# Kernel tuning notes

Hardware: AMD Instinct MI355X
Metric: run time of the kernel (lower is better)

Reference implementation:

```python
import jax, jax.numpy as jnp
import numpy as np
from jax import lax

WINDOW_RADIUS = 8  # model_config['window_radius']


def _layernorm(x, g, b, eps=1e-5):
    mu = jnp.mean(x, axis=-1, keepdims=True)
    var = jnp.var(x, axis=-1, keepdims=True)
    return (x - mu) * lax.rsqrt(var + eps) * g + b


def setup_inputs() -> dict:
    key = jax.random.key(0)
    ks = jax.random.split(key, 8)
    B, T, D = 4, 2048, 1024
    d_b, d_k, KV = 256, 128, 48
    d_in = D + d_b + d_k  # 1408
    s = 1.0 / np.sqrt(D)
    return {
        "h": jax.random.normal(ks[0], (B, T, D), jnp.float32),
        "bound_w": jax.random.normal(ks[1], (D,), jnp.float32) * s,
        "bound_b": jnp.zeros((1,), jnp.float32),
        "conv_w": jax.random.normal(ks[2], (9,), jnp.float32) * (1.0 / 3.0),
        "conv_b": jnp.zeros((1,), jnp.float32),
        "e0": jnp.zeros((d_b,), jnp.float32),
        "e1": jax.random.normal(ks[3], (d_b,), jnp.float32) * 0.02,
        "key_emb": jax.random.normal(ks[4], (KV, d_k), jnp.float32),
        "key_w": jax.random.normal(ks[5], (D, KV), jnp.float32) * s,
        "key_b": jnp.zeros((KV,), jnp.float32),
        "ln_in_g": jnp.ones((d_in,), jnp.float32),
        "ln_in_b": jnp.zeros((d_in,), jnp.float32),
        "film_w": jax.random.normal(ks[6], (d_in, 2 * D), jnp.float32) * (1.0 / np.sqrt(d_in)),
        "film_b": jnp.zeros((2 * D,), jnp.float32),
        "ln_h_g": jnp.ones((D,), jnp.float32),
        "ln_h_b": jnp.zeros((D,), jnp.float32),
    }


def reference(h, bound_w, bound_b, conv_w, conv_b, e0, e1, key_emb, key_w, key_b,
              ln_in_g, ln_in_b, film_w, film_b, ln_h_g, ln_h_b):
    B, T, D = h.shape
    R = WINDOW_RADIUS
    # boundary head + Conv1d(1,1,k,padding=k//2) smoother + sigmoid
    boundary_logits = jnp.einsum('btd,d->bt', h, bound_w) + bound_b[0]  # [B,T]
    kb = conv_w.shape[0]
    sm = lax.conv_general_dilated(boundary_logits[:, None, :], conv_w[None, None, :],
                                  window_strides=(1,), padding=[(kb // 2, kb // 2)])
    b_soft = jax.nn.sigmoid(sm[:, 0, :] + conv_b[0])  # [B,T]
    # key conditioning: softmax over key logits, soft-mix of key embedding table
    key_soft = jax.nn.softmax(jnp.einsum('btd,dk->btk', h, key_w) + key_b, axis=-1)
    ek = jnp.einsum('btk,ke->bte', key_soft, key_emb)  # [B,T,d_k]
    # boundary embedding interpolation
    eb = b_soft[..., None] * e1 + (1.0 - b_soft[..., None]) * e0  # [B,T,d_b]
    # FiLM: concat + LN + Linear -> gamma/beta, modulate LN(h)
    film_in = _layernorm(jnp.concatenate([h, eb, ek], axis=-1), ln_in_g, ln_in_b)
    gb = jnp.einsum('bti,io->bto', film_in, film_w) + film_b  # [B,T,2D]
    gamma, beta = gb[..., :D], gb[..., D:]
    z = _layernorm(h, ln_h_g, ln_h_b) * (1.0 + gamma) + beta  # [B,T,D]
    # local windows: replicate-pad along T, im2col-style gather of width 2R+1
    padded = jnp.pad(h, ((0, 0), (R, R), (0, 0)), mode='edge')  # [B,T+2R,D]
    idx = jnp.arange(T)[:, None] + jnp.arange(2 * R + 1)[None, :]  # [T,W]
    win = padded[:, idx, :]  # [B,T,W,D]
    C = jnp.concatenate([z[:, :, None, :], win], axis=2)  # [B,T,W+1,D]
    return C
```

## Files before the change

kernel.cpp:

```cpp
#include <hip/hip_runtime.h>
#include <math.h>

#define B_    4
#define T_    2048
#define D_    1024
#define DB_   256
#define DKk_  128
#define KV_   48
#define DIN_  1408
#define NT_   (B_ * T_)
#define RAD_  8

#define OFS_BOUND  0
#define OFS_BSOFT  8192
#define OFS_KEY    16384
#define OFS_EK     409600
#define OFS_HSTAT  1458176
#define OFS_BF16   1474560
#define UOFS_AHI   0u
#define UOFS_ALO   11534336u
#define UOFS_BHI   23068672u
#define UOFS_BLO   25952256u

typedef __attribute__((ext_vector_type(8))) short s16x8;
typedef __attribute__((ext_vector_type(4))) float f32x4;

__device__ __forceinline__ unsigned short f2bf(float f) {
    unsigned u; __builtin_memcpy(&u, &f, 4);
    u += 0x7fffu + ((u >> 16) & 1u);
    return (unsigned short)(u >> 16);
}
__device__ __forceinline__ unsigned short f2bf_hi(float f, float* back) {
    unsigned u; __builtin_memcpy(&u, &f, 4);
    u += 0x7fffu + ((u >> 16) & 1u);
    unsigned short h = (unsigned short)(u >> 16);
    unsigned hb = (unsigned)h << 16;
    __builtin_memcpy(back, &hb, 4);
    return h;
}
__device__ __forceinline__ void gload_lds16(const void* g, void* s) {
    __builtin_amdgcn_global_load_lds(
        (const __attribute__((address_space(1))) unsigned int*)g,
        (__attribute__((address_space(3))) unsigned int*)s,
        16, 0, 0);
}

__global__ __launch_bounds__(256) void k_prepw(
    const float* __restrict__ film_w, unsigned short* __restrict__ Bhi,
    unsigned short* __restrict__ Blo)
{
    __shared__ float tile[32][33];
    const int n0 = blockIdx.x * 32;
    const int k0 = blockIdx.y * 32;
    const int tid = threadIdx.x;
    const int c = tid & 31, r0 = tid >> 5;
    #pragma unroll
    for (int i = 0; i < 4; ++i) {
        int r = r0 + i * 8;
        tile[r][c] = film_w[(size_t)(k0 + r) * 2048 + n0 + c];
    }
    __syncthreads();
    #pragma unroll
    for (int i = 0; i < 4; ++i) {
        int rn = r0 + i * 8;
        float f = tile[c][rn];
        float fh;
        unsigned short hs = f2bf_hi(f, &fh);
        unsigned short ls = f2bf(f - fh);
        Bhi[(size_t)(n0 + rn) * 1408 + k0 + c] = hs;
        Blo[(size_t)(n0 + rn) * 1408 + k0 + c] = ls;
    }
}

__global__ __launch_bounds__(256) void k_logits(
    const float* __restrict__ h, const float* __restrict__ bound_w,
    const float* __restrict__ bound_b, const float* __restrict__ key_w,
    const float* __restrict__ key_b, float* __restrict__ ws)
{
    __shared__ float As[32][64];
    __shared__ float Ws[64][64];
    const int tid  = threadIdx.x;
    const int tok0 = blockIdx.x * 32;
    const int c  = tid & 63;
    const int rg = tid >> 6;
    float acc[8] = {0,0,0,0,0,0,0,0};

    for (int kc = 0; kc < 1024; kc += 64) {
        #pragma unroll
        for (int i = 0; i < 8; ++i) {
            int row = rg + 4 * i;
            As[row][c] = h[(size_t)(tok0 + row) * 1024 + kc + c];
        }
        #pragma unroll
        for (int i = 0; i < 12; ++i) {
            int l = tid + 256 * i;
            int r = l / 48, cc = l - r * 48;
            Ws[r][cc] = key_w[(size_t)(kc + r) * 48 + cc];
        }
        if (tid < 64) Ws[tid][48] = bound_w[kc + tid];
        __syncthreads();
        #pragma unroll 8
        for (int kk = 0; kk < 64; ++kk) {
            float w = Ws[kk][c];
            #pragma unroll
            for (int i = 0; i < 8; ++i)
                acc[i] += As[rg * 8 + i][kk] * w;
        }
        __syncthreads();
    }

    if (c < 48) {
        float kb = key_b[c];
        #pragma unroll
        for (int i = 0; i < 8; ++i)
            ws[OFS_KEY + (size_t)(tok0 + rg * 8 + i) * 48 + c] = acc[i] + kb;
    } else if (c == 48) {
        float bb = bound_b[0];
        #pragma unroll
        for (int i = 0; i < 8; ++i)
            ws[OFS_BOUND + tok0 + rg * 8 + i] = acc[i] + bb;
    }
}

__global__ __launch_bounds__(256) void k_conv(
    const float* __restrict__ conv_w, const float* __restrict__ conv_b,
    float* __restrict__ ws)
{
    int id = blockIdx.x * 256 + threadIdx.x;
    if (id >= NT_) return;
    int b = id >> 11, t = id & 2047;
    float s = conv_b[0];
    #pragma unroll
    for (int i = 0; i < 9; ++i) {
        int tt = t + i - 4;
        if (tt >= 0 && tt < T_) s += ws[OFS_BOUND + b * T_ + tt] * conv_w[i];
    }
    ws[OFS_BSOFT + id] = 1.0f / (1.0f + expf(-s));
}

__global__ __launch_bounds__(128) void k_softek(
    const float* __restrict__ key_emb, float* __restrict__ ws)
{
    __shared__ float p[48];
    const int tok = blockIdx.x;
    const int tid = threadIdx.x;
    if (tid < 64) {
        float v = (tid < 48) ? ws[OFS_KEY + (size_t)tok * 48 + tid] : -1e30f;
        float m = v;
        #pragma unroll
        for (int off = 32; off; off >>= 1) m = fmaxf(m, __shfl_xor(m, off, 64));
        float e = (tid < 48) ? expf(v - m) : 0.0f;
        float s = e;
        #pragma unroll
        for (int off = 32; off; off >>= 1) s += __shfl_xor(s, off, 64);
        if (tid < 48) p[tid] = e / s;
    }
    __syncthreads();
    float acc = 0.0f;
    #pragma unroll 8
    for (int k = 0; k < 48; ++k) acc += p[k] * key_emb[k * 128 + tid];
    ws[OFS_EK + (size_t)tok * 128 + tid] = acc;
}

__global__ __launch_bounds__(256) void k_filmin(
    const float* __restrict__ h, const float* __restrict__ e0,
    const float* __restrict__ e1, const float* __restrict__ ln_in_g,
    const float* __restrict__ ln_in_b, float* __restrict__ ws,
    unsigned short* __restrict__ Ahi, unsigned short* __restrict__ Alo)
{
    const int tok = blockIdx.x;
    const int tid = threadIdx.x;
    const float bs = ws[OFS_BSOFT + tok];
    float val[6];
    float s_all = 0.f, ss_all = 0.f, s_h = 0.f, ss_h = 0.f;
    int n = 0;
    for (int j = tid; j < DIN_; j += 256, ++n) {
        float v;
        if (j < 1024)       v = h[(size_t)tok * 1024 + j];
        else if (j < 1280)  { int i = j - 1024; v = bs * e1[i] + (1.0f - bs) * e0[i]; }
        else                v = ws[OFS_EK + (size_t)tok * 128 + (j - 1280)];
        val[n] = v;
        s_all += v; ss_all += v * v;
        if (j < 1024) { s_h += v; ss_h += v * v; }
    }
    #pragma unroll
    for (int off = 32; off; off >>= 1) {
        s_all  += __shfl_down(s_all, off);
        ss_all += __shfl_down(ss_all, off);
        s_h    += __shfl_down(s_h, off);
        ss_h   += __shfl_down(ss_h, off);
    }
    __shared__ float red[4][4];
    const int wid = tid >> 6;
    if ((tid & 63) == 0) {
        red[wid][0] = s_all; red[wid][1] = ss_all;
        red[wid][2] = s_h;   red[wid][3] = ss_h;
    }
    __syncthreads();
    float S   = red[0][0] + red[1][0] + red[2][0] + red[3][0];
    float SS  = red[0][1] + red[1][1] + red[2][1] + red[3][1];
    float Sh  = red[0][2] + red[1][2] + red[2][2] + red[3][2];
    float SSh = red[0][3] + red[1][3] + red[2][3] + red[3][3];
    float mean  = S * (1.0f / 1408.0f);
    float var   = SS * (1.0f / 1408.0f) - mean * mean;
    float rstd  = rsqrtf(var + 1e-5f);
    float mean_h = Sh * (1.0f / 1024.0f);
    float var_h  = SSh * (1.0f / 1024.0f) - mean_h * mean_h;
    float rstd_h = rsqrtf(var_h + 1e-5f);
    if (tid == 0) {
        ws[OFS_HSTAT + tok * 2]     = mean_h;
        ws[OFS_HSTAT + tok * 2 + 1] = rstd_h;
    }
    n = 0;
    for (int j = tid; j < DIN_; j += 256, ++n) {
        float f = (val[n] - mean) * rstd * ln_in_g[j] + ln_in_b[j];
        float fh;
        unsigned short hs = f2bf_hi(f, &fh);
        Ahi[(size_t)tok * 1408 + j] = hs;
        Alo[(size_t)tok * 1408 + j] = f2bf(f - fh);
    }
}

__global__ __launch_bounds__(256) void k_gemm_mfma(
    const unsigned short* __restrict__ Ahi, const unsigned short* __restrict__ Alo,
    const unsigned short* __restrict__ Bhi, const unsigned short* __restrict__ Blo,
    const float* __restrict__ film_b, const float* __restrict__ h,
    const float* __restrict__ hstat, const float* __restrict__ ln_h_g,
    const float* __restrict__ ln_h_b, float* __restrict__ out)
{
    __shared__ __align__(16) char lds[32768];
    const int tid  = threadIdx.x;
    const int m0   = blockIdx.x * 128;
    const int n0   = blockIdx.y * 64;
    const int lane = tid & 63;
    const int wid  = tid >> 6;
    const int wm   = wid >> 1, wn = wid & 1;
    const int lr   = lane & 15;
    const int hi16 = ((lane >> 4) & 3) * 16;
    const int sa   = (lr & 7) << 4;
    const int srow = tid >> 3;
    const int sswz = ((((tid & 7) * 16) ^ ((srow & 7) << 4)) >> 1);
    const int sdst = tid * 16;

    f32x4 accg[4][2] = {};
    f32x4 accb[4][2] = {};

    #pragma unroll
    for (int s = 0; s < 3; ++s) {
        const unsigned short* Ap = (s == 1) ? Alo : Ahi;
        const unsigned short* Bp = (s == 2) ? Blo : Bhi;
        for (int kc = 0; kc < 1408; kc += 64) {
            #pragma unroll
            for (int c = 0; c < 4; ++c)
                gload_lds16(Ap + (size_t)(m0 + srow + c * 32) * 1408 + kc + sswz,
                            lds + c * 4096 + sdst);
            #pragma unroll
            for (int c = 0; c < 2; ++c) {
                gload_lds16(Bp + (size_t)(n0 + srow + c * 32) * 1408 + kc + sswz,
                            lds + 16384 + c * 4096 + sdst);
                gload_lds16(Bp + (size_t)(1024 + n0 + srow + c * 32) * 1408 + kc + sswz,
                            lds + 24576 + c * 4096 + sdst);
            }
            __syncthreads();
            #pragma unroll
            for (int ks = 0; ks < 2; ++ks) {
                s16x8 af[4], bg[2], bb[2];
                #pragma unroll
                for (int mt = 0; mt < 4; ++mt) {
                    int row = wm * 64 + mt * 16 + lr;
                    af[mt] = *(const s16x8*)(lds + row * 128 + ((ks * 64 + hi16) ^ sa));
                }
                #pragma unroll
                for (int nt = 0; nt < 2; ++nt) {
                    int off = (wn * 32 + nt * 16 + lr) * 128 + ((ks * 64 + hi16) ^ sa);
                    bg[nt] = *(const s16x8*)(lds + 16384 + off);
                    bb[nt] = *(const s16x8*)(lds + 24576 + off);
                }
                #pragma unroll
                for (int mt = 0; mt < 4; ++mt)
                    #pragma unroll
                    for (int nt = 0; nt < 2; ++nt) {
                        accg[mt][nt] = __builtin_amdgcn_mfma_f32_16x16x32_bf16(
                            af[mt], bg[nt], accg[mt][nt], 0, 0, 0);
                        accb[mt][nt] = __builtin_amdgcn_mfma_f32_16x16x32_bf16(
                            af[mt], bb[nt], accb[mt][nt], 0, 0, 0);
                    }
            }
            __syncthreads();
        }
    }

    #pragma unroll
    for (int mt = 0; mt < 4; ++mt) {
        #pragma unroll
        for (int r = 0; r < 4; ++r) {
            const int tok = m0 + wm * 64 + mt * 16 + ((lane >> 4) & 3) * 4 + r;
            const float mh = hstat[tok * 2], rh = hstat[tok * 2 + 1];
            #pragma unroll
            for (int nt = 0; nt < 2; ++nt) {
                const int nc = n0 + wn * 32 + nt * 16 + lr;
                float g  = accg[mt][nt][r] + film_b[nc];
                float bt = accb[mt][nt][r] + film_b[1024 + nc];
                float hv = h[(size_t)tok * 1024 + nc];
                float lnh = (hv - mh) * rh * ln_h_g[nc] + ln_h_b[nc];
                out[(size_t)tok * (18 * 1024) + nc] = lnh * (1.0f + g) + bt;
            }
        }
    }
}

__global__ __launch_bounds__(256) void k_window(
    const float* __restrict__ h, float* __restrict__ out)
{
    const int tokg = blockIdx.x;
    const int t = tokg & 2047, b = tokg >> 11;
    float4* dst = (float4*)&out[(size_t)tokg * 18 * 1024];
    #pragma unroll 4
    for (int slot = 0; slot < 17; ++slot) {
        int st = t + slot - RAD_;
        st = st < 0 ? 0 : (st > T_ - 1 ? T_ - 1 : st);
        const float4* src = (const float4*)&h[(size_t)(b * T_ + st) * 1024];
        dst[(1 + slot) * 256 + threadIdx.x] = src[threadIdx.x];
    }
}

extern "C" void kernel_launch(void* const* d_in, const int* in_sizes, int n_in,
                              void* d_out, int out_size, void* d_ws, size_t ws_size,
                              hipStream_t stream)
{
    const float* h       = (const float*)d_in[0];
    const float* bound_w = (const float*)d_in[1];
    const float* bound_b = (const float*)d_in[2];
    const float* conv_w  = (const float*)d_in[3];
    const float* conv_b  = (const float*)d_in[4];
    const float* e0      = (const float*)d_in[5];
    const float* e1      = (const float*)d_in[6];
    const float* key_emb = (const float*)d_in[7];
    const float* key_w   = (const float*)d_in[8];
    const float* key_b   = (const float*)d_in[9];
    const float* ln_in_g = (const float*)d_in[10];
    const float* ln_in_b = (const float*)d_in[11];
    const float* film_w  = (const float*)d_in[12];
    const float* film_b  = (const float*)d_in[13];
    const float* ln_h_g  = (const float*)d_in[14];
    const float* ln_h_b  = (const float*)d_in[15];
    float* ws  = (float*)d_ws;
    float* out = (float*)d_out;
    unsigned short* ub  = (unsigned short*)(ws + OFS_BF16);
    unsigned short* Ahi = ub + UOFS_AHI;
    unsigned short* Alo = ub + UOFS_ALO;
    unsigned short* Bhi = ub + UOFS_BHI;
    unsigned short* Blo = ub + UOFS_BLO;

    hipLaunchKernelGGL(k_prepw, dim3(64, 44), dim3(256), 0, stream,
                       film_w, Bhi, Blo);
    hipLaunchKernelGGL(k_logits, dim3(NT_ / 32), dim3(256), 0, stream,
                       h, bound_w, bound_b, key_w, key_b, ws);
    hipLaunchKernelGGL(k_conv, dim3(NT_ / 256), dim3(256), 0, stream,
                       conv_w, conv_b, ws);
    hipLaunchKernelGGL(k_softek, dim3(NT_), dim3(128), 0, stream, key_emb, ws);
    hipLaunchKernelGGL(k_filmin, dim3(NT_), dim3(256), 0, stream,
                       h, e0, e1, ln_in_g, ln_in_b, ws, Ahi, Alo);
    hipLaunchKernelGGL(k_gemm_mfma, dim3(64, 16), dim3(256), 0, stream,
                       Ahi, Alo, Bhi, Blo, film_b, h, ws + OFS_HSTAT,
                       ln_h_g, ln_h_b, out);
    hipLaunchKernelGGL(k_window, dim3(NT_), dim3(256), 0, stream, h, out);
}
```

Baseline: 949.1 us.

## Merge split-bf16 GEMM passes into one K loop and vectorize logits loads

The three-pass split-bf16 FiLM GEMM (hi*hi, lo*hi, hi*lo) now runs as a single K loop. Ahi and Alo are staged together, Bhi is staged first and then swapped for Blo in the same LDS slot, so the A-hi fragments stay in registers and the A tile is loaded from global memory once instead of three times. LDS per block grows from 32 KB to 48 KB and there are extra barriers, which may lower occupancy. The logits kernel also switches to float4 global and LDS loads, pads the A tile, and unrolls the K loop by four.

```diff
diff --git a/kernel.cpp b/kernel.cpp
--- a/kernel.cpp
+++ b/kernel.cpp
@@ -77,19 +77,23 @@
     const float* __restrict__ bound_b, const float* __restrict__ key_w,
     const float* __restrict__ key_b, float* __restrict__ ws)
 {
-    __shared__ float As[32][64];
+    __shared__ __align__(16) float As[32][68];
     __shared__ float Ws[64][64];
     const int tid  = threadIdx.x;
     const int tok0 = blockIdx.x * 32;
     const int c  = tid & 63;
     const int rg = tid >> 6;
+    const int arow = tid >> 3;
+    const int akb  = (tid & 7) * 8;
     float acc[8] = {0,0,0,0,0,0,0,0};
 
     for (int kc = 0; kc < 1024; kc += 64) {
-        #pragma unroll
-        for (int i = 0; i < 8; ++i) {
-            int row = rg + 4 * i;
-            As[row][c] = h[(size_t)(tok0 + row) * 1024 + kc + c];
+        {
+            const float* src = &h[(size_t)(tok0 + arow) * 1024 + kc + akb];
+            float4 a0 = *(const float4*)(src);
+            float4 a1 = *(const float4*)(src + 4);
+            *(float4*)&As[arow][akb]     = a0;
+            *(float4*)&As[arow][akb + 4] = a1;
         }
         #pragma unroll
         for (int i = 0; i < 12; ++i) {
@@ -99,12 +103,17 @@
         }
         if (tid < 64) Ws[tid][48] = bound_w[kc + tid];
         __syncthreads();
-        #pragma unroll 8
-        for (int kk = 0; kk < 64; ++kk) {
-            float w = Ws[kk][c];
-            #pragma unroll
-            for (int i = 0; i < 8; ++i)
-                acc[i] += As[rg * 8 + i][kk] * w;
+        #pragma unroll
+        for (int kk4 = 0; kk4 < 16; ++kk4) {
+            float w0 = Ws[kk4 * 4 + 0][c];
+            float w1 = Ws[kk4 * 4 + 1][c];
+            float w2 = Ws[kk4 * 4 + 2][c];
+            float w3 = Ws[kk4 * 4 + 3][c];
+            #pragma unroll
+            for (int i = 0; i < 8; ++i) {
+                float4 a = *(const float4*)&As[rg * 8 + i][kk4 * 4];
+                acc[i] += a.x * w0 + a.y * w1 + a.z * w2 + a.w * w3;
+            }
         }
         __syncthreads();
     }
@@ -228,7 +237,7 @@
     const float* __restrict__ hstat, const float* __restrict__ ln_h_g,
     const float* __restrict__ ln_h_b, float* __restrict__ out)
 {
-    __shared__ __align__(16) char lds[32768];
+    __shared__ __align__(16) char lds[49152];
     const int tid  = threadIdx.x;
     const int m0   = blockIdx.x * 128;
     const int n0   = blockIdx.y * 64;
@@ -245,49 +254,85 @@
     f32x4 accg[4][2] = {};
     f32x4 accb[4][2] = {};
 
-    #pragma unroll
-    for (int s = 0; s < 3; ++s) {
-        const unsigned short* Ap = (s == 1) ? Alo : Ahi;
-        const unsigned short* Bp = (s == 2) ? Blo : Bhi;
-        for (int kc = 0; kc < 1408; kc += 64) {
-            #pragma unroll
-            for (int c = 0; c < 4; ++c)
-                gload_lds16(Ap + (size_t)(m0 + srow + c * 32) * 1408 + kc + sswz,
-                            lds + c * 4096 + sdst);
-            #pragma unroll
-            for (int c = 0; c < 2; ++c) {
-                gload_lds16(Bp + (size_t)(n0 + srow + c * 32) * 1408 + kc + sswz,
-                            lds + 16384 + c * 4096 + sdst);
-                gload_lds16(Bp + (size_t)(1024 + n0 + srow + c * 32) * 1408 + kc + sswz,
-                            lds + 24576 + c * 4096 + sdst);
+    for (int kc = 0; kc < 1408; kc += 64) {
+        #pragma unroll
+        for (int c = 0; c < 4; ++c) {
+            gload_lds16(Ahi + (size_t)(m0 + srow + c * 32) * 1408 + kc + sswz,
+                        lds + c * 4096 + sdst);
+            gload_lds16(Alo + (size_t)(m0 + srow + c * 32) * 1408 + kc + sswz,
+                        lds + 16384 + c * 4096 + sdst);
+        }
+        #pragma unroll
+        for (int c = 0; c < 2; ++c) {
+            gload_lds16(Bhi + (size_t)(n0 + srow + c * 32) * 1408 + kc + sswz,
+                        lds + 32768 + c * 4096 + sdst);
+            gload_lds16(Bhi + (size_t)(1024 + n0 + srow + c * 32) * 1408 + kc + sswz,
+                        lds + 40960 + c * 4096 + sdst);
+        }
+        __syncthreads();
+
+        s16x8 afK[2][4];
+        #pragma unroll
+        for (int ks = 0; ks < 2; ++ks) {
+            s16x8 al[4], bg[2], bb[2];
+            #pragma unroll
+            for (int mt = 0; mt < 4; ++mt) {
+                int row = wm * 64 + mt * 16 + lr;
+                int koff = (ks * 64 + hi16) ^ sa;
+                afK[ks][mt] = *(const s16x8*)(lds + row * 128 + koff);
+                al[mt]      = *(const s16x8*)(lds + 16384 + row * 128 + koff);
             }
-            __syncthreads();
-            #pragma unroll
-            for (int ks = 0; ks < 2; ++ks) {
-                s16x8 af[4], bg[2], bb[2];
-                #pragma unroll
-                for (int mt = 0; mt < 4; ++mt) {
-                    int row = wm * 64 + mt * 16 + lr;
-                    af[mt] = *(const s16x8*)(lds + row * 128 + ((ks * 64 + hi16) ^ sa));
-                }
+            #pragma unroll
+            for (int nt = 0; nt < 2; ++nt) {
+                int off = (wn * 32 + nt * 16 + lr) * 128 + ((ks * 64 + hi16) ^ sa);
+                bg[nt] = *(const s16x8*)(lds + 32768 + off);
+                bb[nt] = *(const s16x8*)(lds + 40960 + off);
+            }
+            #pragma unroll
+            for (int mt = 0; mt < 4; ++mt)
                 #pragma unroll
                 for (int nt = 0; nt < 2; ++nt) {
-                    int off = (wn * 32 + nt * 16 + lr) * 128 + ((ks * 64 + hi16) ^ sa);
-                    bg[nt] = *(const s16x8*)(lds + 16384 + off);
-                    bb[nt] = *(const s16x8*)(lds + 24576 + off);
+                    accg[mt][nt] = __builtin_amdgcn_mfma_f32_16x16x32_bf16(
+                        afK[ks][mt], bg[nt], accg[mt][nt], 0, 0, 0);
+                    accg[mt][nt] = __builtin_amdgcn_mfma_f32_16x16x32_bf16(
+                        al[mt], bg[nt], accg[mt][nt], 0, 0, 0);
+                    accb[mt][nt] = __builtin_amdgcn_mfma_f32_16x16x32_bf16(
+                        afK[ks][mt], bb[nt], accb[mt][nt], 0, 0, 0);
+                    accb[mt][nt] = __builtin_amdgcn_mfma_f32_16x16x32_bf16(
+                        al[mt], bb[nt], accb[mt][nt], 0, 0, 0);
                 }
+        }
+        __syncthreads();
+
+        #pragma unroll
+        for (int c = 0; c < 2; ++c) {
+            gload_lds16(Blo + (size_t)(n0 + srow + c * 32) * 1408 + kc + sswz,
+                        lds + 32768 + c * 4096 + sdst);
+            gload_lds16(Blo + (size_t)(1024 + n0 + srow + c * 32) * 1408 + kc + sswz,
+                        lds + 40960 + c * 4096 + sdst);
+        }
+        __syncthreads();
+
+        #pragma unroll
+        for (int ks = 0; ks < 2; ++ks) {
+            s16x8 bg[2], bb[2];
+            #pragma unroll
+            for (int nt = 0; nt < 2; ++nt) {
+                int off = (wn * 32 + nt * 16 + lr) * 128 + ((ks * 64 + hi16) ^ sa);
+                bg[nt] = *(const s16x8*)(lds + 32768 + off);
+                bb[nt] = *(const s16x8*)(lds + 40960 + off);
+            }
+            #pragma unroll
+            for (int mt = 0; mt < 4; ++mt)
                 #pragma unroll
-                for (int mt = 0; mt < 4; ++mt)
-                    #pragma unroll
-                    for (int nt = 0; nt < 2; ++nt) {
-                        accg[mt][nt] = __builtin_amdgcn_mfma_f32_16x16x32_bf16(
-                            af[mt], bg[nt], accg[mt][nt], 0, 0, 0);
-                        accb[mt][nt] = __builtin_amdgcn_mfma_f32_16x16x32_bf16(
-                            af[mt], bb[nt], accb[mt][nt], 0, 0, 0);
-                    }
-            }
-            __syncthreads();
-        }
+                for (int nt = 0; nt < 2; ++nt) {
+                    accg[mt][nt] = __builtin_amdgcn_mfma_f32_16x16x32_bf16(
+                        afK[ks][mt], bg[nt], accg[mt][nt], 0, 0, 0);
+                    accb[mt][nt] = __builtin_amdgcn_mfma_f32_16x16x32_bf16(
+                        afK[ks][mt], bb[nt], accb[mt][nt], 0, 0, 0);
+                }
+        }
+        __syncthreads();
     }
 
     #pragma unroll
```

Result: faster. 909.7 us (-4.1%).

## Double-buffer FiLM GEMM LDS, swizzle workgroups, vectorize logits kernel loads

Applied to the files above, without the earlier changes.

The split-bf16 FiLM GEMM is restructured so that all three hi/lo passes form one flat loop of 66 k-chunks. It uses two 32KB LDS buffers, so the async global-to-LDS load of the next chunk overlaps the MFMA work on the current one, and one barrier per chunk replaces two. The grid becomes 1D with a remapped block index so that consecutive workgroups share B tiles for better L2 reuse. The logits kernel loads h with float4 into a padded LDS tile and reads four k values per vector. The cost is doubled LDS use, which may lower occupancy.

```diff
diff --git a/kernel.cpp b/kernel.cpp
--- a/kernel.cpp
+++ b/kernel.cpp
@@ -77,19 +77,23 @@
     const float* __restrict__ bound_b, const float* __restrict__ key_w,
     const float* __restrict__ key_b, float* __restrict__ ws)
 {
-    __shared__ float As[32][64];
+    __shared__ __align__(16) float As[32][68];
     __shared__ float Ws[64][64];
     const int tid  = threadIdx.x;
     const int tok0 = blockIdx.x * 32;
     const int c  = tid & 63;
     const int rg = tid >> 6;
+    const int arow = tid >> 3;
+    const int akb  = (tid & 7) * 8;
     float acc[8] = {0,0,0,0,0,0,0,0};
 
     for (int kc = 0; kc < 1024; kc += 64) {
-        #pragma unroll
-        for (int i = 0; i < 8; ++i) {
-            int row = rg + 4 * i;
-            As[row][c] = h[(size_t)(tok0 + row) * 1024 + kc + c];
+        {
+            const float* src = &h[(size_t)(tok0 + arow) * 1024 + kc + akb];
+            float4 a0 = *(const float4*)(src);
+            float4 a1 = *(const float4*)(src + 4);
+            *(float4*)&As[arow][akb]     = a0;
+            *(float4*)&As[arow][akb + 4] = a1;
         }
         #pragma unroll
         for (int i = 0; i < 12; ++i) {
@@ -99,12 +103,17 @@
         }
         if (tid < 64) Ws[tid][48] = bound_w[kc + tid];
         __syncthreads();
-        #pragma unroll 8
-        for (int kk = 0; kk < 64; ++kk) {
-            float w = Ws[kk][c];
-            #pragma unroll
-            for (int i = 0; i < 8; ++i)
-                acc[i] += As[rg * 8 + i][kk] * w;
+        #pragma unroll
+        for (int kk4 = 0; kk4 < 16; ++kk4) {
+            float w0 = Ws[kk4 * 4 + 0][c];
+            float w1 = Ws[kk4 * 4 + 1][c];
+            float w2 = Ws[kk4 * 4 + 2][c];
+            float w3 = Ws[kk4 * 4 + 3][c];
+            #pragma unroll
+            for (int i = 0; i < 8; ++i) {
+                float4 a = *(const float4*)&As[rg * 8 + i][kk4 * 4];
+                acc[i] += a.x * w0 + a.y * w1 + a.z * w2 + a.w * w3;
+            }
         }
         __syncthreads();
     }
@@ -228,10 +237,12 @@
     const float* __restrict__ hstat, const float* __restrict__ ln_h_g,
     const float* __restrict__ ln_h_b, float* __restrict__ out)
 {
-    __shared__ __align__(16) char lds[32768];
+    __shared__ __align__(16) char lds[65536];
     const int tid  = threadIdx.x;
-    const int m0   = blockIdx.x * 128;
-    const int n0   = blockIdx.y * 64;
+    const int wg   = blockIdx.x;
+    const int swz  = (wg & 7) * 128 + (wg >> 3);
+    const int m0   = (swz & 63) * 128;
+    const int n0   = (swz >> 6) * 64;
     const int lane = tid & 63;
     const int wid  = tid >> 6;
     const int wm   = wid >> 1, wn = wid & 1;
@@ -245,49 +256,55 @@
     f32x4 accg[4][2] = {};
     f32x4 accb[4][2] = {};
 
-    #pragma unroll
-    for (int s = 0; s < 3; ++s) {
-        const unsigned short* Ap = (s == 1) ? Alo : Ahi;
-        const unsigned short* Bp = (s == 2) ? Blo : Bhi;
-        for (int kc = 0; kc < 1408; kc += 64) {
-            #pragma unroll
-            for (int c = 0; c < 4; ++c)
-                gload_lds16(Ap + (size_t)(m0 + srow + c * 32) * 1408 + kc + sswz,
-                            lds + c * 4096 + sdst);
-            #pragma unroll
-            for (int c = 0; c < 2; ++c) {
-                gload_lds16(Bp + (size_t)(n0 + srow + c * 32) * 1408 + kc + sswz,
-                            lds + 16384 + c * 4096 + sdst);
-                gload_lds16(Bp + (size_t)(1024 + n0 + srow + c * 32) * 1408 + kc + sswz,
-                            lds + 24576 + c * 4096 + sdst);
+    auto stage = [&](int cc, int bufi) {
+        const unsigned short* Ap = (cc < 22) ? Ahi : (cc < 44 ? Alo : Ahi);
+        const unsigned short* Bp = (cc < 44) ? Bhi : Blo;
+        const int kc = (cc >= 44 ? cc - 44 : (cc >= 22 ? cc - 22 : cc)) * 64;
+        char* base = lds + bufi * 32768;
+        #pragma unroll
+        for (int c = 0; c < 4; ++c) {
+            gload_lds16(Ap + (size_t)(m0 + srow + c * 32) * 1408 + kc + sswz,
+                        base + c * 4096 + sdst);
+            int r = srow + c * 32;
+            int col = n0 + r + ((r >> 6) * 960);
+            gload_lds16(Bp + (size_t)col * 1408 + kc + sswz,
+                        base + 16384 + c * 4096 + sdst);
+        }
+    };
+
+    stage(0, 0);
+    __syncthreads();
+
+    for (int cc = 0; cc < 66; ++cc) {
+        const int cur = cc & 1;
+        if (cc + 1 < 66) stage(cc + 1, cur ^ 1);
+        const char* base = lds + cur * 32768;
+        #pragma unroll
+        for (int ks = 0; ks < 2; ++ks) {
+            s16x8 af[4], bg[2], bb[2];
+            const int koff = (ks * 64 + hi16) ^ sa;
+            #pragma unroll
+            for (int mt = 0; mt < 4; ++mt) {
+                int row = wm * 64 + mt * 16 + lr;
+                af[mt] = *(const s16x8*)(base + row * 128 + koff);
             }
-            __syncthreads();
-            #pragma unroll
-            for (int ks = 0; ks < 2; ++ks) {
-                s16x8 af[4], bg[2], bb[2];
-                #pragma unroll
-                for (int mt = 0; mt < 4; ++mt) {
-                    int row = wm * 64 + mt * 16 + lr;
-                    af[mt] = *(const s16x8*)(lds + row * 128 + ((ks * 64 + hi16) ^ sa));
-                }
+            #pragma unroll
+            for (int nt = 0; nt < 2; ++nt) {
+                int rg = wn * 32 + nt * 16 + lr;
+                bg[nt] = *(const s16x8*)(base + 16384 + rg * 128 + koff);
+                bb[nt] = *(const s16x8*)(base + 16384 + (rg + 64) * 128 + koff);
+            }
+            #pragma unroll
+            for (int mt = 0; mt < 4; ++mt)
                 #pragma unroll
                 for (int nt = 0; nt < 2; ++nt) {
-                    int off = (wn * 32 + nt * 16 + lr) * 128 + ((ks * 64 + hi16) ^ sa);
-                    bg[nt] = *(const s16x8*)(lds + 16384 + off);
-                    bb[nt] = *(const s16x8*)(lds + 24576 + off);
+                    accg[mt][nt] = __builtin_amdgcn_mfma_f32_16x16x32_bf16(
+                        af[mt], bg[nt], accg[mt][nt], 0, 0, 0);
+                    accb[mt][nt] = __builtin_amdgcn_mfma_f32_16x16x32_bf16(
+                        af[mt], bb[nt], accb[mt][nt], 0, 0, 0);
                 }
-                #pragma unroll
-                for (int mt = 0; mt < 4; ++mt)
-                    #pragma unroll
-                    for (int nt = 0; nt < 2; ++nt) {
-                        accg[mt][nt] = __builtin_amdgcn_mfma_f32_16x16x32_bf16(
-                            af[mt], bg[nt], accg[mt][nt], 0, 0, 0);
-                        accb[mt][nt] = __builtin_amdgcn_mfma_f32_16x16x32_bf16(
-                            af[mt], bb[nt], accb[mt][nt], 0, 0, 0);
-                    }
-            }
-            __syncthreads();
-        }
+        }
+        __syncthreads();
     }
 
     #pragma unroll
@@ -361,7 +378,7 @@
     hipLaunchKernelGGL(k_softek, dim3(NT_), dim3(128), 0, stream, key_emb, ws);
     hipLaunchKernelGGL(k_filmin, dim3(NT_), dim3(256), 0, stream,
                        h, e0, e1, ln_in_g, ln_in_b, ws, Ahi, Alo);
-    hipLaunchKernelGGL(k_gemm_mfma, dim3(64, 16), dim3(256), 0, stream,
+    hipLaunchKernelGGL(k_gemm_mfma, dim3(1024), dim3(256), 0, stream,
                        Ahi, Alo, Bhi, Blo, film_b, h, ws + OFS_HSTAT,
                        ln_h_g, ln_h_b, out);
     hipLaunchKernelGGL(k_window, dim3(NT_), dim3(256), 0, stream, h, out);
```

Measured after the change: 961.1 us. Within noise of the previous version (+1.3%).
